# Optimization experiments

Measured on AMD Instinct MI355X. Metric: run time of the kernel, lower is better.

The kernel has to match this reference:

```python
import jax, jax.numpy as jnp
import numpy as np

D_MODEL = 2048
NUM_HEADS = 16
D_K = D_MODEL // NUM_HEADS  # 128
BATCH, SEQ = 2, 2048


def setup_inputs() -> dict:
    key = jax.random.key(0)
    ks = jax.random.split(key, 9)
    s = 0.02
    return {
        "x": jax.random.normal(ks[0], (BATCH, SEQ, D_MODEL), dtype=jnp.float32),
        "W_q": jax.random.normal(ks[1], (D_MODEL, D_MODEL), dtype=jnp.float32) * s,
        "b_q": jax.random.normal(ks[2], (D_MODEL,), dtype=jnp.float32) * s,
        "W_k": jax.random.normal(ks[3], (D_MODEL, D_K), dtype=jnp.float32) * s,
        "b_k": jax.random.normal(ks[4], (D_K,), dtype=jnp.float32) * s,
        "W_v": jax.random.normal(ks[5], (D_MODEL, D_K), dtype=jnp.float32) * s,
        "b_v": jax.random.normal(ks[6], (D_K,), dtype=jnp.float32) * s,
        "W_o": jax.random.normal(ks[7], (D_MODEL, D_MODEL), dtype=jnp.float32) * s,
        "b_o": jax.random.normal(ks[8], (D_MODEL,), dtype=jnp.float32) * s,
    }


def reference(x, W_q, b_q, W_k, b_k, W_v, b_v, W_o, b_o):
    B, S, _ = x.shape
    # Q: per-head projections -> (B, H, S, d_k)
    Q = (x @ W_q + b_q).reshape(B, S, NUM_HEADS, D_K).transpose(0, 2, 1, 3)
    # K, V: single shared head -> (B, S, d_k)
    K = x @ W_k + b_k
    V = x @ W_v + b_v
    scale = 1.0 / np.sqrt(D_K)
    # scores: (B, H, S_q, S_k); K broadcast across heads (no expand materialized)
    scores = jnp.einsum("bhqd,bkd->bhqk", Q, K) * scale
    attn = jax.nn.softmax(scores, axis=-1)
    out = jnp.einsum("bhqk,bkd->bhqd", attn, V)  # (B, H, S, d_k)
    out = out.transpose(0, 2, 1, 3).reshape(B, S, D_MODEL)
    out = out @ W_o + b_o
    K_cache = K[:, None, :, :]  # (B, 1, S, d_k)
    V_cache = V[:, None, :, :]
    return (out, K_cache, V_cache)
```

## Files before the change

### kernel.cpp

```cpp
#include <hip/hip_runtime.h>
#include <cstdint>

typedef __bf16 bf16x8 __attribute__((ext_vector_type(8)));
typedef float f32x4 __attribute__((ext_vector_type(4)));
typedef unsigned short ushort_t;

constexpr int kS  = 2048;
constexpr int kDM = 2048;
constexpr int kDK = 128;
constexpr int kNH = 16;
constexpr int kB  = 2;
constexpr int kNQKV = kDM + 2 * kDK;

__device__ __forceinline__ unsigned short f2bf(float f) {
  union { float f; unsigned u; } v; v.f = f;
  unsigned u = v.u;
  u += 0x7fffu + ((u >> 16) & 1u);
  return (unsigned short)(u >> 16);
}

__device__ __forceinline__ void gload16(const void* g, void* l) {
  __builtin_amdgcn_global_load_lds(
      (const __attribute__((address_space(1))) void*)g,
      (__attribute__((address_space(3))) void*)l, 16, 0, 0);
}

__global__ __launch_bounds__(256) void cast_f32_bf16(const float* __restrict__ in,
                                                     ushort_t* __restrict__ out, long n) {
  long i = ((long)blockIdx.x * 256 + threadIdx.x) * 4;
  if (i >= n) return;
  float4 f = *reinterpret_cast<const float4*>(in + i);
  ushort4 o;
  o.x = f2bf(f.x); o.y = f2bf(f.y); o.z = f2bf(f.z); o.w = f2bf(f.w);
  *reinterpret_cast<ushort4*>(out + i) = o;
}

__global__ __launch_bounds__(256) void transpose_cast(const float* __restrict__ in,
                                                      ushort_t* __restrict__ out,
                                                      int R, int C) {
  __shared__ float tile[32][33];
  int c = blockIdx.x * 32 + threadIdx.x;
  int r0 = blockIdx.y * 32;
  #pragma unroll
  for (int i = threadIdx.y; i < 32; i += 8)
    tile[i][threadIdx.x] = in[(long)(r0 + i) * C + c];
  __syncthreads();
  int oc  = r0 + threadIdx.x;
  int or0 = blockIdx.x * 32;
  #pragma unroll
  for (int i = threadIdx.y; i < 32; i += 8)
    out[(long)(or0 + i) * R + oc] = f2bf(tile[threadIdx.x][i]);
}

__device__ __forceinline__ void gemm128(const ushort_t* __restrict__ A, int lda,
                                        const ushort_t* __restrict__ Bt, int ldb,
                                        int K, int row0, int col0,
                                        f32x4 (&acc)[4][4]) {
  __shared__ __align__(16) ushort_t sA[128 * 32];
  __shared__ __align__(16) ushort_t sB[128 * 32];
  int t = threadIdx.x;
  int r = t >> 2, c4 = t & 3;
  const ushort_t* gA0 = A  + (long)(row0 + r)      * lda + c4 * 8;
  const ushort_t* gA1 = A  + (long)(row0 + r + 64) * lda + c4 * 8;
  const ushort_t* gB0 = Bt + (long)(col0 + r)      * ldb + c4 * 8;
  const ushort_t* gB1 = Bt + (long)(col0 + r + 64) * ldb + c4 * 8;
  int lane = t & 63, wave = t >> 6;
  int wr = wave >> 1, wc = wave & 1;
  int lr = lane & 15, lg = lane >> 4;
  int aoff = (wr * 64 + lr) * 32 + lg * 8;
  int boff = (wc * 64 + lr) * 32 + lg * 8;

  for (int kk = 0; kk < K; kk += 32) {
    gload16(gA0 + kk, (void*)(sA + t * 8));
    gload16(gA1 + kk, (void*)(sA + 2048 + t * 8));
    gload16(gB0 + kk, (void*)(sB + t * 8));
    gload16(gB1 + kk, (void*)(sB + 2048 + t * 8));
    __syncthreads();
    bf16x8 af[4], bg[4];
    #pragma unroll
    for (int i = 0; i < 4; i++) af[i] = *(const bf16x8*)(sA + aoff + i * 16 * 32);
    #pragma unroll
    for (int j = 0; j < 4; j++) bg[j] = *(const bf16x8*)(sB + boff + j * 16 * 32);
    #pragma unroll
    for (int i = 0; i < 4; i++)
      #pragma unroll
      for (int j = 0; j < 4; j++)
        acc[i][j] = __builtin_amdgcn_mfma_f32_16x16x32_bf16(af[i], bg[j], acc[i][j], 0, 0, 0);
    __syncthreads();
  }
}

__global__ __launch_bounds__(256) void gemm_qkv(const ushort_t* __restrict__ x,
    const ushort_t* __restrict__ Wt, const float* __restrict__ bq,
    const float* __restrict__ bk, const float* __restrict__ bv,
    ushort_t* __restrict__ Qb, float* __restrict__ Kc,
    ushort_t* __restrict__ Kb, float* __restrict__ Vc, ushort_t* __restrict__ Vtb) {
  f32x4 acc[4][4] = {};
  int row0 = blockIdx.y * 128, col0 = blockIdx.x * 128;
  gemm128(x, kDM, Wt, kDM, kDM, row0, col0, acc);
  int lane = threadIdx.x & 63, wave = threadIdx.x >> 6;
  int wr = wave >> 1, wc = wave & 1, lr = lane & 15, lg = lane >> 4;
  #pragma unroll
  for (int i = 0; i < 4; i++) {
    #pragma unroll
    for (int j = 0; j < 4; j++) {
      int col = col0 + wc * 64 + j * 16 + lr;
      float bias = (col < kDM) ? bq[col]
                 : (col < kDM + kDK) ? bk[col - kDM] : bv[col - kDM - kDK];
      #pragma unroll
      for (int rr = 0; rr < 4; rr++) {
        int row = row0 + wr * 64 + i * 16 + lg * 4 + rr;
        float v = acc[i][j][rr] + bias;
        if (col < kDM) {
          Qb[(long)row * kDM + col] = f2bf(v);
        } else if (col < kDM + kDK) {
          int c = col - kDM;
          Kc[(long)row * kDK + c] = v;
          Kb[(long)row * kDK + c] = f2bf(v);
        } else {
          int c = col - kDM - kDK;
          Vc[(long)row * kDK + c] = v;
          Vtb[((long)(row >> 11) * kDK + c) * kS + (row & 2047)] = f2bf(v);
        }
      }
    }
  }
}

__global__ __launch_bounds__(256) void gemm_out(const ushort_t* __restrict__ A,
    const ushort_t* __restrict__ Wt, const float* __restrict__ bias,
    float* __restrict__ C) {
  f32x4 acc[4][4] = {};
  int row0 = blockIdx.y * 128, col0 = blockIdx.x * 128;
  gemm128(A, kDM, Wt, kDM, kDM, row0, col0, acc);
  int lane = threadIdx.x & 63, wave = threadIdx.x >> 6;
  int wr = wave >> 1, wc = wave & 1, lr = lane & 15, lg = lane >> 4;
  #pragma unroll
  for (int i = 0; i < 4; i++) {
    #pragma unroll
    for (int j = 0; j < 4; j++) {
      int col = col0 + wc * 64 + j * 16 + lr;
      float bv = bias[col];
      #pragma unroll
      for (int rr = 0; rr < 4; rr++) {
        int row = row0 + wr * 64 + i * 16 + lg * 4 + rr;
        C[(long)row * kDM + col] = acc[i][j][rr] + bv;
      }
    }
  }
}

__global__ __launch_bounds__(256, 2) void flash_attn(
    const ushort_t* __restrict__ Qb, const ushort_t* __restrict__ Kb,
    const ushort_t* __restrict__ Vt, ushort_t* __restrict__ Ob) {
  __shared__ __align__(16) ushort_t sK[2][64 * 128];
  __shared__ __align__(16) ushort_t sV[2][64 * 128];

  const int tid = threadIdx.x;
  const int L = tid & 63, wave = tid >> 6;
  const int lr = L & 15, lg = L >> 4;
  const int bh = blockIdx.y, b = bh >> 4, h = bh & 15;
  const int q0 = blockIdx.x * 128;

  const ushort_t* Kg = Kb + (long)b * kS * kDK;
  const ushort_t* Vg = Vt + (long)b * kDK * kS;
  const ushort_t* Qg = Qb + ((long)b * kS + q0 + wave * 32) * kDM + h * kDK;

  bf16x8 qf[2][4];
  #pragma unroll
  for (int i = 0; i < 2; i++)
    #pragma unroll
    for (int kk = 0; kk < 4; kk++)
      qf[i][kk] = *(const bf16x8*)(Qg + (long)(i * 16 + lr) * kDM + kk * 32 + lg * 8);

  int koff[4], voff[4];
  #pragma unroll
  for (int s = 0; s < 4; s++) {
    int c = tid + s * 256;
    int f = c >> 6, cl = c & 63;
    int st = f >> 2, kk = f & 3, n = cl & 15;
    int key = (st >> 1) * 32 + (n >> 2) * 8 + (st & 1) * 4 + (n & 3);
    koff[s] = key * kDK + kk * 32 + (cl >> 4) * 8;
    int d = c >> 3, kb = (c & 7) ^ (d & 7);
    voff[s] = d * kS + kb * 8;
  }

  f32x4 accO[8][2] = {};
  float lsum[2] = {};

  constexpr float kScaleLog2e = 0.12751743f;

  auto stage = [&](int jt, int bb) {
    const ushort_t* Kt = Kg + (long)jt * 64 * kDK;
    const ushort_t* Vtg = Vg + jt * 64;
    #pragma unroll
    for (int s = 0; s < 4; s++) {
      int c8 = (tid + s * 256) * 8;
      gload16(Kt + koff[s], (void*)(sK[bb] + c8));
      gload16(Vtg + voff[s], (void*)(sV[bb] + c8));
    }
  };

  auto compute = [&](int bb) {
    #pragma unroll
    for (int u = 0; u < 2; u++) {
      f32x4 sacc[2][2] = {};
      __builtin_amdgcn_s_setprio(1);
      #pragma unroll
      for (int kk = 0; kk < 4; kk++)
        #pragma unroll
        for (int jj = 0; jj < 2; jj++) {
          bf16x8 kf = *(const bf16x8*)(sK[bb] + ((u * 2 + jj) * 4 + kk) * 512 + L * 8);
          #pragma unroll
          for (int i = 0; i < 2; i++)
            sacc[jj][i] = __builtin_amdgcn_mfma_f32_16x16x32_bf16(kf, qf[i][kk], sacc[jj][i], 0, 0, 0);
        }
      __builtin_amdgcn_s_setprio(0);

      bf16x8 pf[2];
      #pragma unroll
      for (int i = 0; i < 2; i++) {
        union { bf16x8 v; unsigned w[4]; } P;
        #pragma unroll
        for (int jj = 0; jj < 2; jj++) {
          float p0 = __builtin_amdgcn_exp2f(sacc[jj][i][0] * kScaleLog2e);
          float p1 = __builtin_amdgcn_exp2f(sacc[jj][i][1] * kScaleLog2e);
          float p2 = __builtin_amdgcn_exp2f(sacc[jj][i][2] * kScaleLog2e);
          float p3 = __builtin_amdgcn_exp2f(sacc[jj][i][3] * kScaleLog2e);
          lsum[i] += (p0 + p1) + (p2 + p3);
          asm("v_cvt_pk_bf16_f32 %0, %1, %2" : "=v"(P.w[jj * 2 + 0]) : "v"(p0), "v"(p1));
          asm("v_cvt_pk_bf16_f32 %0, %1, %2" : "=v"(P.w[jj * 2 + 1]) : "v"(p2), "v"(p3));
        }
        pf[i] = P.v;
      }

      __builtin_amdgcn_s_setprio(1);
      #pragma unroll
      for (int t = 0; t < 8; t++) {
        int kbL = (u * 4 + lg) ^ (lr & 7);
        bf16x8 vf = *(const bf16x8*)(sV[bb] + t * 1024 + lr * 64 + kbL * 8);
        #pragma unroll
        for (int i = 0; i < 2; i++)
          accO[t][i] = __builtin_amdgcn_mfma_f32_16x16x32_bf16(vf, pf[i], accO[t][i], 0, 0, 0);
      }
      __builtin_amdgcn_s_setprio(0);
    }
  };

  stage(0, 0);
  __syncthreads();
  for (int jt = 0; jt < 32; jt += 2) {
    stage(jt + 1, 1);
    compute(0);
    __syncthreads();
    if (jt + 2 < 32) stage(jt + 2, 0);
    compute(1);
    __syncthreads();
  }

  float inv[2];
  #pragma unroll
  for (int i = 0; i < 2; i++) {
    float v = lsum[i];
    v += __shfl_xor(v, 16);
    v += __shfl_xor(v, 32);
    inv[i] = 1.0f / v;
  }

  ushort_t* Og = Ob + ((long)b * kS + q0 + wave * 32) * kDM + h * kDK;
  #pragma unroll
  for (int t = 0; t < 8; t++)
    #pragma unroll
    for (int i = 0; i < 2; i++) {
      union { ushort4 o; unsigned w[2]; } O;
      float f0 = accO[t][i][0] * inv[i];
      float f1 = accO[t][i][1] * inv[i];
      float f2 = accO[t][i][2] * inv[i];
      float f3 = accO[t][i][3] * inv[i];
      asm("v_cvt_pk_bf16_f32 %0, %1, %2" : "=v"(O.w[0]) : "v"(f0), "v"(f1));
      asm("v_cvt_pk_bf16_f32 %0, %1, %2" : "=v"(O.w[1]) : "v"(f2), "v"(f3));
      *(ushort4*)(Og + (long)(i * 16 + lr) * kDM + t * 16 + lg * 4) = O.o;
    }
}

extern "C" void kernel_launch(void* const* d_in, const int* in_sizes, int n_in,
                              void* d_out, int out_size, void* d_ws, size_t ws_size,
                              hipStream_t stream) {
  (void)in_sizes; (void)n_in; (void)out_size; (void)ws_size;
  const float* x   = (const float*)d_in[0];
  const float* W_q = (const float*)d_in[1];
  const float* b_q = (const float*)d_in[2];
  const float* W_k = (const float*)d_in[3];
  const float* b_k = (const float*)d_in[4];
  const float* W_v = (const float*)d_in[5];
  const float* b_v = (const float*)d_in[6];
  const float* W_o = (const float*)d_in[7];
  const float* b_o = (const float*)d_in[8];

  float* out = (float*)d_out;
  float* Kc  = out + (long)kB * kS * kDM;
  float* Vc  = Kc  + (long)kB * kS * kDK;

  char* w = (char*)d_ws;
  ushort_t* x_bf   = (ushort_t*)w;  w += 16777216;
  ushort_t* Wall_t = (ushort_t*)w;  w += (size_t)kNQKV*kDM*2;
  ushort_t* Wo_t   = (ushort_t*)w;  w += 8388608;
  ushort_t* Q_bf   = (ushort_t*)w;  w += 16777216;
  ushort_t* K_bf   = (ushort_t*)w;  w += 1048576;
  ushort_t* Vt_bf  = (ushort_t*)w;  w += 1048576;
  ushort_t* O_bf   = (ushort_t*)w;  w += 16777216;

  dim3 blk(256);
  dim3 tblk(32, 8);

  cast_f32_bf16<<<dim3(8192), blk, 0, stream>>>(x, x_bf, (long)kB * kS * kDM);
  transpose_cast<<<dim3(64, 64), tblk, 0, stream>>>(W_q, Wall_t, kDM, kDM);
  transpose_cast<<<dim3(4, 64),  tblk, 0, stream>>>(W_k, Wall_t + (long)kDM * kDM, kDM, kDK);
  transpose_cast<<<dim3(4, 64),  tblk, 0, stream>>>(W_v, Wall_t + (long)(kDM + kDK) * kDM, kDM, kDK);
  transpose_cast<<<dim3(64, 64), tblk, 0, stream>>>(W_o, Wo_t, kDM, kDM);

  gemm_qkv<<<dim3(kNQKV / 128, kB * kS / 128), blk, 0, stream>>>(
      x_bf, Wall_t, b_q, b_k, b_v, Q_bf, Kc, K_bf, Vc, Vt_bf);

  flash_attn<<<dim3(kS / 128, kB * kNH), blk, 0, stream>>>(Q_bf, K_bf, Vt_bf, O_bf);

  gemm_out<<<dim3(kDM / 128, kB * kS / 128), blk, 0, stream>>>(O_bf, Wo_t, b_o, out);
}
```

Baseline: 313.6 us.

## Double-buffer GEMM LDS tiles and swizzle blocks across XCDs

The shared GEMM core now uses two LDS buffers and issues the async global-to-LDS loads for the next K slice before computing on the current one, so memory latency can overlap with MFMA work. Both projection GEMMs also remap block indices so that consecutive blocks land on the same XCD, improving L2 reuse of shared A/B tiles. This doubles LDS use per block, which may reduce occupancy, and the swizzle assumes the block count is a multiple of eight.

```diff
diff --git a/kernel.cpp b/kernel.cpp
--- a/kernel.cpp
+++ b/kernel.cpp
@@ -23,6 +23,16 @@
   __builtin_amdgcn_global_load_lds(
       (const __attribute__((address_space(1))) void*)g,
       (__attribute__((address_space(3))) void*)l, 16, 0, 0);
+}
+
+__device__ __forceinline__ void xcd_swizzle(int& bx, int& by) {
+  int gx = gridDim.x;
+  int nwg = gx * gridDim.y;
+  int id = by * gx + bx;
+  int cpx = nwg >> 3;
+  int sw = (id & 7) * cpx + (id >> 3);
+  bx = sw % gx;
+  by = sw / gx;
 }
 
 __global__ __launch_bounds__(256) void cast_f32_bf16(const float* __restrict__ in,
@@ -56,8 +66,8 @@
                                         const ushort_t* __restrict__ Bt, int ldb,
                                         int K, int row0, int col0,
                                         f32x4 (&acc)[4][4]) {
-  __shared__ __align__(16) ushort_t sA[128 * 32];
-  __shared__ __align__(16) ushort_t sB[128 * 32];
+  __shared__ __align__(16) ushort_t sA[2][128 * 32];
+  __shared__ __align__(16) ushort_t sB[2][128 * 32];
   int t = threadIdx.x;
   int r = t >> 2, c4 = t & 3;
   const ushort_t* gA0 = A  + (long)(row0 + r)      * lda + c4 * 8;
@@ -70,22 +80,33 @@
   int aoff = (wr * 64 + lr) * 32 + lg * 8;
   int boff = (wc * 64 + lr) * 32 + lg * 8;
 
-  for (int kk = 0; kk < K; kk += 32) {
-    gload16(gA0 + kk, (void*)(sA + t * 8));
-    gload16(gA1 + kk, (void*)(sA + 2048 + t * 8));
-    gload16(gB0 + kk, (void*)(sB + t * 8));
-    gload16(gB1 + kk, (void*)(sB + 2048 + t * 8));
-    __syncthreads();
+  auto stage = [&](int kk, int bb) {
+    gload16(gA0 + kk, (void*)(sA[bb] + t * 8));
+    gload16(gA1 + kk, (void*)(sA[bb] + 2048 + t * 8));
+    gload16(gB0 + kk, (void*)(sB[bb] + t * 8));
+    gload16(gB1 + kk, (void*)(sB[bb] + 2048 + t * 8));
+  };
+  auto comp = [&](int bb) {
     bf16x8 af[4], bg[4];
     #pragma unroll
-    for (int i = 0; i < 4; i++) af[i] = *(const bf16x8*)(sA + aoff + i * 16 * 32);
-    #pragma unroll
-    for (int j = 0; j < 4; j++) bg[j] = *(const bf16x8*)(sB + boff + j * 16 * 32);
+    for (int i = 0; i < 4; i++) af[i] = *(const bf16x8*)(sA[bb] + aoff + i * 16 * 32);
+    #pragma unroll
+    for (int j = 0; j < 4; j++) bg[j] = *(const bf16x8*)(sB[bb] + boff + j * 16 * 32);
     #pragma unroll
     for (int i = 0; i < 4; i++)
       #pragma unroll
       for (int j = 0; j < 4; j++)
         acc[i][j] = __builtin_amdgcn_mfma_f32_16x16x32_bf16(af[i], bg[j], acc[i][j], 0, 0, 0);
+  };
+
+  stage(0, 0);
+  __syncthreads();
+  for (int kk = 0; kk < K; kk += 64) {
+    stage(kk + 32, 1);
+    comp(0);
+    __syncthreads();
+    if (kk + 64 < K) stage(kk + 64, 0);
+    comp(1);
     __syncthreads();
   }
 }
@@ -96,7 +117,9 @@
     ushort_t* __restrict__ Qb, float* __restrict__ Kc,
     ushort_t* __restrict__ Kb, float* __restrict__ Vc, ushort_t* __restrict__ Vtb) {
   f32x4 acc[4][4] = {};
-  int row0 = blockIdx.y * 128, col0 = blockIdx.x * 128;
+  int bx = blockIdx.x, by = blockIdx.y;
+  xcd_swizzle(bx, by);
+  int row0 = by * 128, col0 = bx * 128;
   gemm128(x, kDM, Wt, kDM, kDM, row0, col0, acc);
   int lane = threadIdx.x & 63, wave = threadIdx.x >> 6;
   int wr = wave >> 1, wc = wave & 1, lr = lane & 15, lg = lane >> 4;
@@ -131,7 +154,9 @@
     const ushort_t* __restrict__ Wt, const float* __restrict__ bias,
     float* __restrict__ C) {
   f32x4 acc[4][4] = {};
-  int row0 = blockIdx.y * 128, col0 = blockIdx.x * 128;
+  int bx = blockIdx.x, by = blockIdx.y;
+  xcd_swizzle(bx, by);
+  int row0 = by * 128, col0 = bx * 128;
   gemm128(A, kDM, Wt, kDM, kDM, row0, col0, acc);
   int lane = threadIdx.x & 63, wave = threadIdx.x >> 6;
   int wr = wave >> 1, wc = wave & 1, lr = lane & 15, lg = lane >> 4;
```

After: 313.1 us. About the same (-0.2%).
